# Optimization experiments

Hardware: AMD Instinct MI355X
Metric: run time of the kernel (lower is better)

The kernel has to match this reference:

```python
import jax, jax.numpy as jnp
import numpy as np

N_NODES = 100000
N_EDGES = 1600000
NUM_GRAPHS = 128
FLAVOURS = 17
C = 32


def setup_inputs() -> dict:
    key = jax.random.key(0)
    ks = jax.random.split(key, 12)
    return {
        "x_idx": jax.random.randint(ks[0], (N_NODES,), 0, FLAVOURS),
        "edge_index": jax.random.randint(ks[1], (2, N_EDGES), 0, N_NODES),
        "batch": jnp.sort(jax.random.randint(ks[2], (N_NODES,), 0, NUM_GRAPHS)),
        "embed_w": jax.random.normal(ks[3], (FLAVOURS, C), jnp.float32),
        "conv_w": jax.random.normal(ks[4], (5, C, C), jnp.float32) * 0.2,
        "conv_b": jax.random.normal(ks[5], (5, C), jnp.float32) * 0.1,
        "d0_w": jax.random.normal(ks[6], (C, C), jnp.float32) * 0.2,
        "d0_b": jax.random.normal(ks[7], (C,), jnp.float32) * 0.1,
        "dense_w": jax.random.normal(ks[8], (3, C, C), jnp.float32) * 0.2,
        "dense_b": jax.random.normal(ks[9], (3, C), jnp.float32) * 0.1,
        "fin_w": jax.random.normal(ks[10], (2, C), jnp.float32) * 0.2,
        "fin_b": jax.random.normal(ks[11], (2,), jnp.float32) * 0.1,
    }


def reference(x_idx, edge_index, batch, embed_w, conv_w, conv_b,
              d0_w, d0_b, dense_w, dense_b, fin_w, fin_b):
    n = x_idx.shape[0]
    loops = jnp.arange(n)
    src = jnp.concatenate([edge_index[0], loops])  # message sources (x_j)
    dst = jnp.concatenate([edge_index[1], loops])  # aggregation targets
    # GCN symmetric normalization with self-loops: deg^-1/2 A_hat deg^-1/2
    deg = jax.ops.segment_sum(jnp.ones_like(dst, dtype=jnp.float32), dst,
                              num_segments=n)
    dinv = jax.lax.rsqrt(deg)  # deg >= 1 thanks to self-loops
    norm = dinv[src] * dinv[dst]  # [E+N]

    h = embed_w[x_idx]  # [N, C]
    for l in range(5):
        z = h @ conv_w[l].T                      # linear transform
        msgs = norm[:, None] * z[src]            # gather + scale
        agg = jax.ops.segment_sum(msgs, dst, num_segments=n) + conv_b[l]
        h = jax.nn.relu(agg)                     # dropout is identity in eval

    pooled = jax.ops.segment_max(h, batch, num_segments=NUM_GRAPHS)  # [G, C]
    pooled = jnp.where(jnp.isfinite(pooled), pooled, 0.0)  # guard empty graphs

    y = jax.nn.relu(pooled @ d0_w.T + d0_b)
    for l in range(3):
        y = jax.nn.relu(y @ dense_w[l].T + dense_b[l])
    logits = y @ fin_w.T + fin_b  # [G, 2]
    return jax.nn.log_softmax(logits, axis=1)
```

## Files before the change

### kernel.cpp

```cpp
#include <hip/hip_runtime.h>
#include <hip/hip_bf16.h>
#include <hip/hip_fp16.h>


#define CDIM 32
#define BSHIFT 7
#define BSPAN 128
#define MAXBUK 800
#define CHUNK 12800
#define BCAP 2560
#define CSRCAP 3072
#define PCHUNK 128

__global__ void __launch_bounds__(256) bin_count(
    const int* __restrict__ edst, int* __restrict__ counts,
    unsigned* __restrict__ pooled, int E, int nbuk, int G) {
    __shared__ int hist[MAXBUK];
    int t = threadIdx.x;
    if (blockIdx.x == 0) {
        for (int i = t; i < G * CDIM; i += 256) pooled[i] = 0u;
    }
    int base = blockIdx.x * CHUNK;
    int n = min(CHUNK, E - base);
    for (int i = t; i < nbuk; i += 256) hist[i] = 0;
    __syncthreads();
    for (int i = t; i < n; i += 256)
        atomicAdd(&hist[edst[base + i] >> BSHIFT], 1);
    __syncthreads();
    for (int b = t; b < nbuk; b += 256)
        counts[blockIdx.x * MAXBUK + b] = hist[b];
}

__global__ void __launch_bounds__(256) colscan(
    const int* __restrict__ counts, int* __restrict__ runpre,
    int* __restrict__ btot, int nchunks) {
    __shared__ int s[256];
    int b = blockIdx.x, t = threadIdx.x;
    int v = (t < nchunks) ? counts[t * MAXBUK + b] : 0;
    s[t] = v;
    __syncthreads();
    for (int d = 1; d < 256; d <<= 1) {
        int x = (t >= d) ? s[t - d] : 0;
        __syncthreads();
        s[t] += x;
        __syncthreads();
    }
    if (t < nchunks) runpre[t * MAXBUK + b] = s[t] - v;
    if (t == 255) btot[b] = s[255];
}

__global__ void __launch_bounds__(256) bin_scatter(
    const int* __restrict__ esrc, const int* __restrict__ edst,
    const int* __restrict__ runpre, unsigned* __restrict__ pairs,
    int E, int nbuk) {
    __shared__ int lcur[MAXBUK];
    int t = threadIdx.x;
    int base = blockIdx.x * CHUNK;
    int n = min(CHUNK, E - base);
    for (int b = t; b < nbuk; b += 256)
        lcur[b] = runpre[blockIdx.x * MAXBUK + b];
    __syncthreads();
    for (int i = t; i < n; i += 256) {
        int d = edst[base + i];
        int s = esrc[base + i];
        int b = d >> BSHIFT;
        int pos = atomicAdd(&lcur[b], 1);
        pairs[(size_t)b * BCAP + pos] =
            ((unsigned)(d & (BSPAN - 1)) << 20) | (unsigned)s;
    }
}

__global__ void __launch_bounds__(256) build_csr_embed(
    const unsigned* __restrict__ pairs, const int* __restrict__ btot,
    const int* __restrict__ x_idx, const float* __restrict__ ew,
    int* __restrict__ cnt, float* __restrict__ dinvx,
    int* __restrict__ offsets4, int* __restrict__ csr,
    __half* __restrict__ hA, __half* __restrict__ hB, int N) {
    __shared__ int h[BSPAN];
    __shared__ int p[BSPAN];
    __shared__ int lcur[BSPAN];
    __shared__ int obase[BSPAN];
    __shared__ int xi[BSPAN];
    int b = blockIdx.x, t = threadIdx.x;
    int v0 = b << BSHIFT;
    if (t < BSPAN) h[t] = 0;
    __syncthreads();
    size_t p0 = (size_t)b * BCAP;
    size_t p1 = p0 + btot[b];
    for (size_t i = p0 + t; i < p1; i += 256)
        atomicAdd(&h[pairs[i] >> 20], 1);
    __syncthreads();
    int own = 0;
    if (t < BSPAN) {
        int v = v0 + t;
        int c = (v < N) ? h[t] : 0;
        float dv = rsqrtf((float)c + 1.0f);
        if (v < N) {
            cnt[v] = c;
            dinvx[v] = dv;
            xi[t] = x_idx[v];
        }
        h[t] = __float_as_int(dv);
        own = (c + 3) & ~3;
        p[t] = own;
    }
    __syncthreads();
    for (int d = 1; d < BSPAN; d <<= 1) {
        int x = 0;
        if (t < BSPAN && t >= d) x = p[t - d];
        __syncthreads();
        if (t < BSPAN) p[t] += x;
        __syncthreads();
    }
    if (t < BSPAN) {
        int o = b * CSRCAP + p[t] - own;
        int v = v0 + t;
        if (v < N) offsets4[v] = o;
        lcur[t] = o;
        obase[t] = o;
    }
    __syncthreads();
    for (size_t i = p0 + t; i < p1; i += 256) {
        unsigned pk = pairs[i];
        int pos = atomicAdd(&lcur[pk >> 20], 1);
        csr[pos] = (int)(pk & 0xFFFFFu);
    }
    __syncthreads();
    if (t < BSPAN) {
        int v = v0 + t;
        if (v < N) {
            int e = lcur[t];
            int e1 = obase[t] + ((e - obase[t] + 3) & ~3);
            for (; e < e1; ++e) csr[e] = N;
        }
    }
    for (int idx = t; idx < BSPAN * CDIM; idx += 256) {
        int dl = idx >> 5;
        int v = v0 + dl;
        if (v < N) {
            float dv = __int_as_float(h[dl]);
            hA[v * CDIM + (idx & 31)] =
                __float2half(dv * ew[xi[dl] * CDIM + (idx & 31)]);
        }
    }
    if (b == 0 && t < CDIM) {
        dinvx[N] = 0.f;
        hA[N * CDIM + t] = __float2half(0.f);
        hB[N * CDIM + t] = __float2half(0.f);
    }
}

__global__ void __launch_bounds__(256) gcn_layer(
    const __half* __restrict__ ht, const float* __restrict__ dinvx,
    const int* __restrict__ offsets4, const int* __restrict__ cnt,
    const int* __restrict__ csr, const float* __restrict__ W,
    const float* __restrict__ bias, __half* __restrict__ out,
    int N, int scale_next) {
    int c = threadIdx.x & 31;
    int grp = threadIdx.x >> 5;

    float w[CDIM];
    {
        const float4* Wrow = reinterpret_cast<const float4*>(W + c * CDIM);
        #pragma unroll
        for (int q = 0; q < CDIM / 4; ++q) {
            float4 t = Wrow[q];
            w[4 * q + 0] = t.x;
            w[4 * q + 1] = t.y;
            w[4 * q + 2] = t.z;
            w[4 * q + 3] = t.w;
        }
    }
    float bc = bias[c];

    for (int v0 = blockIdx.x * 8; v0 < N; v0 += gridDim.x * 8) {
        int v = v0 + grp;
        if (v >= N) continue;
        float dv = dinvx[v];
        float acc = __half2float(ht[v * CDIM + c]);
        int e = offsets4[v];
        int e1 = e + ((cnt[v] + 3) & ~3);
        for (; e < e1; e += 4) {
            int4 s4 = *reinterpret_cast<const int4*>(&csr[e]);
            float a0 = __half2float(ht[s4.x * CDIM + c]);
            float a1 = __half2float(ht[s4.y * CDIM + c]);
            float a2 = __half2float(ht[s4.z * CDIM + c]);
            float a3 = __half2float(ht[s4.w * CDIM + c]);
            acc += (a0 + a1) + (a2 + a3);
        }
        float aggv = dv * acc;
        float o = bc;
        #pragma unroll
        for (int k = 0; k < CDIM; ++k)
            o = fmaf(__shfl(aggv, k, 32), w[k], o);
        o = fmaxf(o, 0.f);
        if (scale_next) o *= dv;
        out[v * CDIM + c] = __float2half(o);
    }
}

__global__ void pool_kernel(const __half* __restrict__ h, const int* __restrict__ batch,
                            unsigned* __restrict__ pooled, int N) {
    __shared__ int sb[8 * PCHUNK];
    int t = threadIdx.x;
    int chunk0 = blockIdx.x * 8;
    int sbase = chunk0 * PCHUNK;
    for (int i = t; i < 8 * PCHUNK; i += 256)
        sb[i] = (sbase + i < N) ? batch[sbase + i] : -1;
    __syncthreads();
    int c = t & 31, cs = t >> 5;
    int i0 = (chunk0 + cs) * PCHUNK;
    if (i0 >= N) return;
    int curg = sb[cs * PCHUNK];
    float m = -1.0f;
    for (int k = 0; k < PCHUNK; ++k) {
        int i = i0 + k;
        if (i >= N) break;
        int g = sb[cs * PCHUNK + k];
        float v = __half2float(h[i * CDIM + c]);
        if (g != curg) {
            if (m >= 0.f) atomicMax(&pooled[curg * CDIM + c], __float_as_uint(m));
            curg = g;
            m = v;
        } else {
            m = fmaxf(m, v);
        }
    }
    if (m >= 0.f && curg >= 0) atomicMax(&pooled[curg * CDIM + c], __float_as_uint(m));
}

__global__ void __launch_bounds__(256) head_kernel(
    const float* __restrict__ pooled,
    const float* __restrict__ d0_w, const float* __restrict__ d0_b,
    const float* __restrict__ dense_w, const float* __restrict__ dense_b,
    const float* __restrict__ fin_w, const float* __restrict__ fin_b,
    float* __restrict__ out, int G) {
    int c = threadIdx.x & 31;
    int grp = threadIdx.x >> 5;
    int g = blockIdx.x * 8 + grp;
    if (g >= G) return;

    float x = pooled[g * CDIM + c];

    const float* Ws[4] = {d0_w, dense_w, dense_w + CDIM * CDIM,
                          dense_w + 2 * CDIM * CDIM};
    const float* bs[4] = {d0_b, dense_b, dense_b + CDIM, dense_b + 2 * CDIM};
    for (int l = 0; l < 4; ++l) {
        float w[CDIM];
        const float4* Wrow = reinterpret_cast<const float4*>(Ws[l] + c * CDIM);
        #pragma unroll
        for (int q = 0; q < CDIM / 4; ++q) {
            float4 t = Wrow[q];
            w[4 * q + 0] = t.x;
            w[4 * q + 1] = t.y;
            w[4 * q + 2] = t.z;
            w[4 * q + 3] = t.w;
        }
        float acc = bs[l][c];
        #pragma unroll
        for (int k = 0; k < CDIM; ++k)
            acc = fmaf(__shfl(x, k, 32), w[k], acc);
        x = fmaxf(acc, 0.f);
    }
    float p0 = x * fin_w[c];
    float p1 = x * fin_w[CDIM + c];
    #pragma unroll
    for (int d = 16; d > 0; d >>= 1) {
        p0 += __shfl_xor(p0, d, 32);
        p1 += __shfl_xor(p1, d, 32);
    }
    float l0 = p0 + fin_b[0], l1 = p1 + fin_b[1];
    float mm = fmaxf(l0, l1);
    float lse = mm + logf(expf(l0 - mm) + expf(l1 - mm));
    if (c == 0) {
        out[g * 2 + 0] = l0 - lse;
        out[g * 2 + 1] = l1 - lse;
    }
}

extern "C" void kernel_launch(void* const* d_in, const int* in_sizes, int n_in,
                              void* d_out, int out_size, void* d_ws, size_t ws_size,
                              hipStream_t stream) {
    const int* x_idx = (const int*)d_in[0];
    const int* eidx = (const int*)d_in[1];
    const int* batch = (const int*)d_in[2];
    const float* embed_w = (const float*)d_in[3];
    const float* conv_w = (const float*)d_in[4];
    const float* conv_b = (const float*)d_in[5];
    const float* d0_w = (const float*)d_in[6];
    const float* d0_b = (const float*)d_in[7];
    const float* dense_w = (const float*)d_in[8];
    const float* dense_b = (const float*)d_in[9];
    const float* fin_w = (const float*)d_in[10];
    const float* fin_b = (const float*)d_in[11];

    int N = in_sizes[0];
    int E = in_sizes[1] / 2;
    int G = out_size / 2;
    const int* esrc = eidx;
    const int* edst = eidx + E;
    int nbuk = (N + BSPAN - 1) >> BSHIFT;
    int CB = (E + CHUNK - 1) / CHUNK;

    char* ws = (char*)d_ws;
    size_t off = 0;
    auto take = [&](size_t bytes) -> char* {
        char* p = ws + off;
        off = (off + bytes + 255) & ~(size_t)255;
        return p;
    };
    int* cnt = (int*)take((size_t)N * 4);
    float* dinvx = (float*)take((size_t)(N + 1) * 4);
    int* offsets4 = (int*)take((size_t)N * 4);
    int* btot = (int*)take(MAXBUK * 4);
    int* counts = (int*)take((size_t)CB * MAXBUK * 4);
    int* runpre = (int*)take((size_t)CB * MAXBUK * 4);
    unsigned* pairs = (unsigned*)take((size_t)MAXBUK * BCAP * 4);
    int* csr = (int*)take((size_t)MAXBUK * CSRCAP * 4);
    __half* hA = (__half*)take((size_t)(N + 1) * CDIM * 2);
    __half* hB = (__half*)take((size_t)(N + 1) * CDIM * 2);
    unsigned* pooled = (unsigned*)take((size_t)G * CDIM * 4);
    (void)ws_size;
    (void)n_in;

    bin_count<<<CB, 256, 0, stream>>>(edst, counts, pooled, E, nbuk, G);
    colscan<<<nbuk, 256, 0, stream>>>(counts, runpre, btot, CB);
    bin_scatter<<<CB, 256, 0, stream>>>(esrc, edst, runpre, pairs, E, nbuk);
    build_csr_embed<<<nbuk, 256, 0, stream>>>(pairs, btot, x_idx, embed_w,
                                              cnt, dinvx, offsets4, csr, hA, hB, N);

    int LB = 2048;
    gcn_layer<<<LB, 256, 0, stream>>>(hA, dinvx, offsets4, cnt, csr,
                                      conv_w + 0 * CDIM * CDIM, conv_b + 0 * CDIM, hB, N, 1);
    gcn_layer<<<LB, 256, 0, stream>>>(hB, dinvx, offsets4, cnt, csr,
                                      conv_w + 1 * CDIM * CDIM, conv_b + 1 * CDIM, hA, N, 1);
    gcn_layer<<<LB, 256, 0, stream>>>(hA, dinvx, offsets4, cnt, csr,
                                      conv_w + 2 * CDIM * CDIM, conv_b + 2 * CDIM, hB, N, 1);
    gcn_layer<<<LB, 256, 0, stream>>>(hB, dinvx, offsets4, cnt, csr,
                                      conv_w + 3 * CDIM * CDIM, conv_b + 3 * CDIM, hA, N, 1);
    gcn_layer<<<LB, 256, 0, stream>>>(hA, dinvx, offsets4, cnt, csr,
                                      conv_w + 4 * CDIM * CDIM, conv_b + 4 * CDIM, hB, N, 0);

    int nchunks = (N + PCHUNK - 1) / PCHUNK;
    pool_kernel<<<(nchunks + 7) / 8, 256, 0, stream>>>(hB, batch, pooled, N);
    head_kernel<<<(G + 7) / 8, 256, 0, stream>>>((const float*)pooled, d0_w, d0_b,
                                                 dense_w, dense_b, fin_w, fin_b,
                                                 (float*)d_out, G);
}
```

Baseline: 313.6 us.

## Compute first GCN layer via per-node flavour histograms instead of feature gather

The first layer's input is a one-hot embedding lookup, so the aggregation becomes a per-destination weighted histogram over the 17 flavours. Each source contributes its dinv scaled by its packed flavour id. The histogram is then multiplied by the precomputed W·embedding table (32x17) in shared memory. This replaces gathering 32-channel half rows per edge with a single 4-byte packed read plus a shared-memory atomic. It also drops the embedding write from CSR construction. The cost is that dinv is stored as half in the packed word, which slightly reduces precision, and each block recomputes the small W·E product.

```diff
diff --git a/kernel.cpp b/kernel.cpp
--- a/kernel.cpp
+++ b/kernel.cpp
@@ -11,6 +11,7 @@
 #define BCAP 2560
 #define CSRCAP 3072
 #define PCHUNK 128
+#define NFLAV 17
 
 __global__ void __launch_bounds__(256) bin_count(
     const int* __restrict__ edst, int* __restrict__ counts,
@@ -72,15 +73,15 @@
 
 __global__ void __launch_bounds__(256) build_csr_embed(
     const unsigned* __restrict__ pairs, const int* __restrict__ btot,
-    const int* __restrict__ x_idx, const float* __restrict__ ew,
+    const int* __restrict__ x_idx,
     int* __restrict__ cnt, float* __restrict__ dinvx,
+    unsigned* __restrict__ packed,
     int* __restrict__ offsets4, int* __restrict__ csr,
     __half* __restrict__ hA, __half* __restrict__ hB, int N) {
     __shared__ int h[BSPAN];
     __shared__ int p[BSPAN];
     __shared__ int lcur[BSPAN];
     __shared__ int obase[BSPAN];
-    __shared__ int xi[BSPAN];
     int b = blockIdx.x, t = threadIdx.x;
     int v0 = b << BSHIFT;
     if (t < BSPAN) h[t] = 0;
@@ -98,9 +99,9 @@
         if (v < N) {
             cnt[v] = c;
             dinvx[v] = dv;
-            xi[t] = x_idx[v];
-        }
-        h[t] = __float_as_int(dv);
+            packed[v] = (unsigned)__half_as_ushort(__float2half(dv)) |
+                        ((unsigned)x_idx[v] << 16);
+        }
         own = (c + 3) & ~3;
         p[t] = own;
     }
@@ -134,19 +135,71 @@
             for (; e < e1; ++e) csr[e] = N;
         }
     }
-    for (int idx = t; idx < BSPAN * CDIM; idx += 256) {
-        int dl = idx >> 5;
-        int v = v0 + dl;
-        if (v < N) {
-            float dv = __int_as_float(h[dl]);
-            hA[v * CDIM + (idx & 31)] =
-                __float2half(dv * ew[xi[dl] * CDIM + (idx & 31)]);
-        }
-    }
     if (b == 0 && t < CDIM) {
-        dinvx[N] = 0.f;
+        if (t == 0) {
+            dinvx[N] = 0.f;
+            packed[N] = 0u;
+        }
         hA[N * CDIM + t] = __float2half(0.f);
         hB[N * CDIM + t] = __float2half(0.f);
+    }
+}
+
+__global__ void __launch_bounds__(256) gcn_layer1(
+    const unsigned* __restrict__ pairs, const int* __restrict__ btot,
+    const unsigned* __restrict__ packed,
+    const float* __restrict__ W1, const float* __restrict__ b1,
+    const float* __restrict__ ew, __half* __restrict__ out, int N) {
+    __shared__ float WE[CDIM * NFLAV];
+    __shared__ float tt[BSPAN * NFLAV];
+    __shared__ float dvs[BSPAN];
+    int t = threadIdx.x;
+    int b = blockIdx.x;
+    int v0 = b << BSHIFT;
+
+    for (int i = t; i < CDIM * NFLAV; i += 256) {
+        int c = i / NFLAV, f = i % NFLAV;
+        float a = 0.f;
+        #pragma unroll
+        for (int k = 0; k < CDIM; ++k)
+            a += W1[c * CDIM + k] * ew[f * CDIM + k];
+        WE[i] = a;
+    }
+    for (int i = t; i < BSPAN * NFLAV; i += 256) tt[i] = 0.f;
+    __syncthreads();
+    if (t < BSPAN) {
+        int v = v0 + t;
+        float dv = 0.f;
+        if (v < N) {
+            unsigned pk = packed[v];
+            dv = __half2float(__ushort_as_half((unsigned short)(pk & 0xFFFFu)));
+            tt[t * NFLAV + (pk >> 16)] = dv;
+        }
+        dvs[t] = dv;
+    }
+    __syncthreads();
+    size_t p0 = (size_t)b * BCAP;
+    size_t p1 = p0 + btot[b];
+    for (size_t i = p0 + t; i < p1; i += 256) {
+        unsigned pk = pairs[i];
+        int dl = (int)(pk >> 20);
+        unsigned sp = packed[pk & 0xFFFFFu];
+        float dv = __half2float(__ushort_as_half((unsigned short)(sp & 0xFFFFu)));
+        atomicAdd(&tt[dl * NFLAV + (sp >> 16)], dv);
+    }
+    __syncthreads();
+    int c = t & 31, grp = t >> 5;
+    for (int j = 0; j < 16; ++j) {
+        int dl = grp * 16 + j;
+        int v = v0 + dl;
+        if (v >= N) break;
+        float dv = dvs[dl];
+        float s = 0.f;
+        #pragma unroll
+        for (int f = 0; f < NFLAV; ++f)
+            s = fmaf(tt[dl * NFLAV + f], WE[c * NFLAV + f], s);
+        float o = fmaxf(fmaf(dv, s, b1[c]), 0.f) * dv;
+        out[v * CDIM + c] = __float2half(o);
     }
 }
 
@@ -311,6 +364,7 @@
     };
     int* cnt = (int*)take((size_t)N * 4);
     float* dinvx = (float*)take((size_t)(N + 1) * 4);
+    unsigned* packed = (unsigned*)take((size_t)(N + 1) * 4);
     int* offsets4 = (int*)take((size_t)N * 4);
     int* btot = (int*)take(MAXBUK * 4);
     int* counts = (int*)take((size_t)CB * MAXBUK * 4);
@@ -326,12 +380,15 @@
     bin_count<<<CB, 256, 0, stream>>>(edst, counts, pooled, E, nbuk, G);
     colscan<<<nbuk, 256, 0, stream>>>(counts, runpre, btot, CB);
     bin_scatter<<<CB, 256, 0, stream>>>(esrc, edst, runpre, pairs, E, nbuk);
-    build_csr_embed<<<nbuk, 256, 0, stream>>>(pairs, btot, x_idx, embed_w,
-                                              cnt, dinvx, offsets4, csr, hA, hB, N);
+    build_csr_embed<<<nbuk, 256, 0, stream>>>(pairs, btot, x_idx,
+                                              cnt, dinvx, packed,
+                                              offsets4, csr, hA, hB, N);
+
+    gcn_layer1<<<nbuk, 256, 0, stream>>>(pairs, btot, packed,
+                                         conv_w + 0 * CDIM * CDIM,
+                                         conv_b + 0 * CDIM, embed_w, hB, N);
 
     int LB = 2048;
-    gcn_layer<<<LB, 256, 0, stream>>>(hA, dinvx, offsets4, cnt, csr,
-                                      conv_w + 0 * CDIM * CDIM, conv_b + 0 * CDIM, hB, N, 1);
     gcn_layer<<<LB, 256, 0, stream>>>(hB, dinvx, offsets4, cnt, csr,
                                       conv_w + 1 * CDIM * CDIM, conv_b + 1 * CDIM, hA, N, 1);
     gcn_layer<<<LB, 256, 0, stream>>>(hA, dinvx, offsets4, cnt, csr,
```

New measurement: 296.5 us. -5.5%, faster.
